# Performance work log

Measured on AMD Instinct MI355X. Metric: run time of the kernel, lower is better.

The kernel has to match this reference:

```python
import jax, jax.numpy as jnp
import numpy as np

B, N, KEY_DIM, VALUE_DIM, INNER_DIM, HEADS = 2, 4096, 512, 512, 512, 8
DIM_HEAD = INNER_DIM // HEADS
LN_EPS = 1e-5


def _layernorm(x, gamma, beta):
    mu = jnp.mean(x, axis=-1, keepdims=True)
    xc = x - mu
    var = jnp.mean(xc * xc, axis=-1, keepdims=True)
    return xc * jax.lax.rsqrt(var + LN_EPS) * gamma + beta


def setup_inputs() -> dict:
    key = jax.random.key(0)
    ks = jax.random.split(key, 8)
    keys = jax.random.normal(ks[0], (B, N, KEY_DIM), dtype=jnp.float32)
    values = jax.random.normal(ks[1], (B, N, VALUE_DIM), dtype=jnp.float32)
    mask = jax.random.randint(ks[2], (B, N), 0, 2).astype(jnp.bool_)
    W_qk = jax.random.normal(ks[3], (KEY_DIM, 2 * INNER_DIM), dtype=jnp.float32) * 0.02
    W_v = jax.random.normal(ks[4], (VALUE_DIM, INNER_DIM), dtype=jnp.float32) * 0.02
    W_out = jax.random.normal(ks[5], (INNER_DIM, VALUE_DIM), dtype=jnp.float32) * 0.02
    b_out = jnp.zeros((VALUE_DIM,), dtype=jnp.float32)
    qk_gamma = jnp.ones((KEY_DIM,), dtype=jnp.float32)
    qk_beta = jnp.zeros((KEY_DIM,), dtype=jnp.float32)
    v_gamma = jnp.ones((VALUE_DIM,), dtype=jnp.float32)
    v_beta = jnp.zeros((VALUE_DIM,), dtype=jnp.float32)
    return {"keys": keys, "values": values, "mask": mask,
            "qk_gamma": qk_gamma, "qk_beta": qk_beta,
            "v_gamma": v_gamma, "v_beta": v_beta,
            "W_qk": W_qk, "W_v": W_v, "W_out": W_out, "b_out": b_out}


def reference(keys, values, mask, qk_gamma, qk_beta, v_gamma, v_beta, W_qk, W_v, W_out, b_out):
    # LayerNorms on inputs
    kn = _layernorm(keys, qk_gamma, qk_beta)          # [B,N,KEY_DIM]
    vn = _layernorm(values, v_gamma, v_beta)          # [B,N,VALUE_DIM]
    # joint q/k projection, no bias
    qk = kn @ W_qk                                    # [B,N,2*INNER]
    q, k = qk[..., :INNER_DIM], qk[..., INNER_DIM:]
    # split heads: b n (h d) -> b h n d
    q = q.reshape(B, N, HEADS, DIM_HEAD).transpose(0, 2, 1, 3)
    k = k.reshape(B, N, HEADS, DIM_HEAD).transpose(0, 2, 1, 3)
    v = (vn @ W_v).reshape(B, N, HEADS, DIM_HEAD).transpose(0, 2, 1, 3)
    # clamp then scaled QK^T (AttentionMap math)
    q = jnp.clip(q, -5.0, 5.0)
    k = jnp.clip(k, -5.0, 5.0)
    scale = DIM_HEAD ** -0.5
    dots = jnp.einsum("bhqd,bhkd->bhqk", q, k) * scale  # [B,H,N,N]
    # mask: True keys are not attended to; broadcast (B,N)->(B,1,1,N)
    dots = jnp.where(mask[:, None, None, :], -jnp.inf, dots)
    attn = jax.nn.softmax(dots, axis=-1)
    out = jnp.einsum("bhqk,bhkd->bhqd", attn, v)       # [B,H,N,D]
    out = out.transpose(0, 2, 1, 3).reshape(B, N, INNER_DIM)
    return out @ W_out + b_out                         # [B,N,VALUE_DIM]
```

## Files before the change

### kernel.cpp

```cpp
#include <hip/hip_runtime.h>
#include <stdint.h>

typedef float f32x4 __attribute__((ext_vector_type(4)));
typedef float f32x16 __attribute__((ext_vector_type(16)));
typedef short s16x8 __attribute__((ext_vector_type(8)));
typedef int i32x4 __attribute__((ext_vector_type(4)));

typedef const __attribute__((address_space(1))) uint32_t* gas_t;
typedef __attribute__((address_space(3))) uint32_t* las_t;

__device__ __forceinline__ void gload16(const void* g, void* l) {
  __builtin_amdgcn_global_load_lds((gas_t)g, (las_t)l, 16, 0, 0);
}

__device__ __forceinline__ short f2bf(float f) {
  union { float f; uint32_t u; } v; v.f = f;
  uint32_t r = v.u + 0x7fffu + ((v.u >> 16) & 1u);
  return (short)(r >> 16);
}

__device__ __forceinline__ uint32_t cvtpk_bf16(float lo, float hi) {
  uint32_t r;
  asm("v_cvt_pk_bf16_f32 %0, %1, %2" : "=v"(r) : "v"(lo), "v"(hi));
  return r;
}

__device__ __forceinline__ void perm32swap(uint32_t& a, uint32_t& b) {
  asm("v_permlane32_swap_b32 %0, %1" : "+v"(a), "+v"(b));
}

#define MFMA16(a,b,c) __builtin_amdgcn_mfma_f32_16x16x32_bf16((a),(b),(c),0,0,0)
#define MFMA32(a,b,c) __builtin_amdgcn_mfma_f32_32x32x16_bf16((a),(b),(c),0,0,0)

__global__ __launch_bounds__(256) void prep_kernel(
    const uint32_t* __restrict__ maskp,
    const float* __restrict__ W_qk, const float* __restrict__ W_v,
    const float* __restrict__ W_out,
    short* __restrict__ WqkT, short* __restrict__ WvT, short* __restrict__ WoutT,
    const float* __restrict__ keys, const float* __restrict__ values,
    const float* __restrict__ g0, const float* __restrict__ b0,
    const float* __restrict__ g1, const float* __restrict__ b1,
    short* __restrict__ kn, short* __restrict__ vn,
    int* __restrict__ idx, int* __restrict__ cnts) {
  __shared__ float tile[32][33];
  __shared__ int wt[4];
  __shared__ int wdet[4];
  const int bid = blockIdx.x, t = threadIdx.x;
  const int lane = t & 63, w = t >> 6;

  if (bid < 2) {
    const int b = bid;
    uint4 probe = ((const uint4*)maskp)[t];
    bool big = (probe.x > 1u) || (probe.y > 1u) || (probe.z > 1u) || (probe.w > 1u);
    unsigned long long bal = __ballot(big);
    if (lane == 0) wdet[w] = (bal != 0ull) ? 1 : 0;
    __syncthreads();
    const int f = wdet[0] | wdet[1] | wdet[2] | wdet[3];

    int v[16]; int s = 0;
    if (f) {
      uint4 raw = ((const uint4*)((const uint8_t*)maskp + (size_t)b * 4096))[t];
      uint32_t ws_[4] = {raw.x, raw.y, raw.z, raw.w};
#pragma unroll
      for (int e = 0; e < 16; e++)
        v[e] = (((ws_[e >> 2] >> ((e & 3) * 8)) & 0xffu) == 0) ? 1 : 0;
    } else {
#pragma unroll
      for (int j = 0; j < 4; j++) {
        uint4 raw = ((const uint4*)(maskp + (size_t)b * 4096))[t * 4 + j];
        v[j * 4 + 0] = (raw.x == 0); v[j * 4 + 1] = (raw.y == 0);
        v[j * 4 + 2] = (raw.z == 0); v[j * 4 + 3] = (raw.w == 0);
      }
    }
#pragma unroll
    for (int e = 0; e < 16; e++) s += v[e];
    int sc = s;
#pragma unroll
    for (int off = 1; off < 64; off <<= 1) {
      int y = __shfl_up(sc, off);
      if (lane >= off) sc += y;
    }
    if (lane == 63) wt[w] = sc;
    __syncthreads();
    int woff = 0;
#pragma unroll
    for (int i = 0; i < 4; i++) if (i < w) woff += wt[i];
    int base = woff + sc - s;
#pragma unroll
    for (int e = 0; e < 16; e++)
      if (v[e]) { idx[b * 4096 + base] = b * 4096 + t * 16 + e; base++; }
    const int cnt = wt[0] + wt[1] + wt[2] + wt[3];
    const int cpad = (cnt + 127) & ~127;
    for (int j = cnt + t; j < cpad; j += 256) idx[b * 4096 + j] = 8192;
    if (t == 0) { cnts[b * 2] = cnt; cnts[b * 2 + 1] = cpad; }
  } else if (bid < 1026) {
    int job = bid - 2;
    const float* W; short* WT; int C;
    if (job < 512)       { W = W_qk;  WT = WqkT;  C = 1024; }
    else if (job < 768)  { job -= 512; W = W_v;   WT = WvT;  C = 512; }
    else                 { job -= 768; W = W_out; WT = WoutT; C = 512; }
    const int tx_ = C >> 5;
    const int c0 = (job % tx_) * 32, r0 = (job / tx_) * 32;
    const int tx = t & 31, ty = t >> 5;
#pragma unroll
    for (int i = 0; i < 32; i += 8)
      tile[ty + i][tx] = W[(size_t)(r0 + ty + i) * C + c0 + tx];
    __syncthreads();
#pragma unroll
    for (int i = 0; i < 32; i += 8)
      WT[(size_t)(c0 + ty + i) * 512 + r0 + tx] = f2bf(tile[tx][ty + i]);
  } else {
    int job = (bid - 1026) * 4 + w;
    if (job >= 16386) return;
    const int sel = job & 1, row = job >> 1;
    short* out = (sel ? vn : kn) + (size_t)row * 512;
    if (row == 8192) {
      s16x8 z = (s16x8){0,0,0,0,0,0,0,0};
      *(s16x8*)(out + lane * 8) = z;
      return;
    }
    const float* x = (sel ? values : keys) + (size_t)row * 512;
    const float* ga = sel ? g1 : g0;
    const float* be = sel ? b1 : b0;
    float4 a = ((const float4*)x)[lane * 2];
    float4 c = ((const float4*)x)[lane * 2 + 1];
    float s = a.x + a.y + a.z + a.w + c.x + c.y + c.z + c.w;
    float sq = a.x*a.x + a.y*a.y + a.z*a.z + a.w*a.w + c.x*c.x + c.y*c.y + c.z*c.z + c.w*c.w;
#pragma unroll
    for (int m = 1; m < 64; m <<= 1) { s += __shfl_xor(s, m); sq += __shfl_xor(sq, m); }
    float mu = s * (1.0f / 512.0f);
    float var = sq * (1.0f / 512.0f) - mu * mu;
    float rs = rsqrtf(var + 1e-5f);
    float xs[8] = {a.x, a.y, a.z, a.w, c.x, c.y, c.z, c.w};
    s16x8 o;
#pragma unroll
    for (int j = 0; j < 8; j++)
      o[j] = f2bf((xs[j] - mu) * rs * ga[lane * 8 + j] + be[lane * 8 + j]);
    *(s16x8*)(out + lane * 8) = o;
  }
}

__device__ __forceinline__ void gemm_core64(const short* __restrict__ A,
                                            const short* __restrict__ BT,
                                            int row0, int col0,
                                            short* ldsA, short* ldsB,
                                            f32x4 acc[4][2]) {
  const int t = threadIdx.x;
  const int lane = t & 63, w = t >> 6;
  const int wr = w >> 1, wc = w & 1;
  const int l15 = lane & 15, l4 = lane >> 4;
#pragma unroll
  for (int mi = 0; mi < 4; mi++)
#pragma unroll
    for (int ni = 0; ni < 2; ni++) acc[mi][ni] = (f32x4){0.f, 0.f, 0.f, 0.f};

  for (int k0 = 0; k0 < 512; k0 += 64) {
    __syncthreads();
#pragma unroll
    for (int i = 0; i < 4; i++) {
      int q = i * 256 + t;
      int row = q >> 3, ch = q & 7;
      int chs = ch ^ (row & 7);
      gload16(A + (size_t)(row0 + row) * 512 + k0 + chs * 8, ldsA + (i * 256 + w * 64) * 8);
    }
#pragma unroll
    for (int i = 0; i < 2; i++) {
      int q = i * 256 + t;
      int row = q >> 3, ch = q & 7;
      int chs = ch ^ (row & 7);
      gload16(BT + (size_t)(col0 + row) * 512 + k0 + chs * 8, ldsB + (i * 256 + w * 64) * 8);
    }
    __syncthreads();
#pragma unroll
    for (int kk = 0; kk < 2; kk++) {
      s16x8 af[4], bf[2];
#pragma unroll
      for (int mi = 0; mi < 4; mi++) {
        int row = wr * 64 + mi * 16 + l15;
        int ch = (kk * 4 + l4) ^ (row & 7);
        af[mi] = *(const s16x8*)(ldsA + row * 64 + ch * 8);
      }
#pragma unroll
      for (int ni = 0; ni < 2; ni++) {
        int row = wc * 32 + ni * 16 + l15;
        int ch = (kk * 4 + l4) ^ (row & 7);
        bf[ni] = *(const s16x8*)(ldsB + row * 64 + ch * 8);
      }
#pragma unroll
      for (int mi = 0; mi < 4; mi++)
#pragma unroll
        for (int ni = 0; ni < 2; ni++)
          acc[mi][ni] = MFMA16(af[mi], bf[ni], acc[mi][ni]);
    }
  }
}

__device__ __forceinline__ void gemm_core_idx(const short* __restrict__ A,
                                              const short* __restrict__ BT,
                                              const int* __restrict__ idxp,
                                              int row0, int col0,
                                              short* ldsA, short* ldsB,
                                              f32x4 acc[4][4]) {
  const int t = threadIdx.x;
  const int lane = t & 63, w = t >> 6;
  const int wr = w >> 1, wc = w & 1;
  const int l15 = lane & 15, l4 = lane >> 4;
  int arow[4];
#pragma unroll
  for (int i = 0; i < 4; i++)
    arow[i] = idxp[row0 + ((i * 256 + t) >> 3)];
#pragma unroll
  for (int mi = 0; mi < 4; mi++)
#pragma unroll
    for (int ni = 0; ni < 4; ni++) acc[mi][ni] = (f32x4){0.f, 0.f, 0.f, 0.f};

  for (int k0 = 0; k0 < 512; k0 += 64) {
    __syncthreads();
#pragma unroll
    for (int i = 0; i < 4; i++) {
      int q = i * 256 + t;
      int row = q >> 3, ch = q & 7;
      int chs = ch ^ (row & 7);
      gload16(A + (size_t)arow[i] * 512 + k0 + chs * 8, ldsA + (i * 256 + w * 64) * 8);
      gload16(BT + (size_t)(col0 + row) * 512 + k0 + chs * 8, ldsB + (i * 256 + w * 64) * 8);
    }
    __syncthreads();
#pragma unroll
    for (int kk = 0; kk < 2; kk++) {
      s16x8 af[4], bf[4];
#pragma unroll
      for (int mi = 0; mi < 4; mi++) {
        int row = wr * 64 + mi * 16 + l15;
        int ch = (kk * 4 + l4) ^ (row & 7);
        af[mi] = *(const s16x8*)(ldsA + row * 64 + ch * 8);
      }
#pragma unroll
      for (int ni = 0; ni < 4; ni++) {
        int row = wc * 64 + ni * 16 + l15;
        int ch = (kk * 4 + l4) ^ (row & 7);
        bf[ni] = *(const s16x8*)(ldsB + row * 64 + ch * 8);
      }
#pragma unroll
      for (int mi = 0; mi < 4; mi++)
#pragma unroll
        for (int ni = 0; ni < 4; ni++)
          acc[mi][ni] = MFMA16(af[mi], bf[ni], acc[mi][ni]);
    }
  }
}

__global__ __launch_bounds__(256) void proj_kernel(const short* __restrict__ kn,
    const short* __restrict__ vn, const short* __restrict__ WqkT,
    const short* __restrict__ WvT, const int* __restrict__ idx,
    const int* __restrict__ cnts, short* __restrict__ Qg,
    short* __restrict__ Kg, short* __restrict__ VTg) {
  __shared__ short lds[2][128 * 64];
  const int bid = blockIdx.x;
  const int t = threadIdx.x, lane = t & 63, w = t >> 6, wr = w >> 1, wc = w & 1;
  const int l15 = lane & 15, l4 = lane >> 4;

  if (bid < 512) {
    const int bm = bid >> 3, bn = bid & 7;
    f32x4 acc[4][2];
    gemm_core64(kn, WqkT, bm * 128, bn * 64, lds[0], lds[1], acc);
    const float QSCL = 0.125f * 1.44269504088896f;
#pragma unroll
    for (int mi = 0; mi < 4; mi++)
#pragma unroll
      for (int ni = 0; ni < 2; ni++) {
        int c = bn * 64 + wc * 32 + ni * 16 + l15;
        int h = c >> 6, d = c & 63;
#pragma unroll
        for (int r = 0; r < 4; r++) {
          int row = bm * 128 + wr * 64 + mi * 16 + l4 * 4 + r;
          int b = row >> 12, n = row & 4095;
          float v = acc[mi][ni][r];
          v = fminf(fmaxf(v, -5.0f), 5.0f) * QSCL;
          Qg[((size_t)((b * 8 + h) * 4096 + n) << 6) + d] = f2bf(v);
        }
      }
  } else {
    const int b2 = bid - 512;
    const int bm = b2 >> 4, bn = (b2 >> 2) & 3, z = b2 & 3;
    const int b = z & 1, isV = z >> 1;
    if (bm * 128 >= cnts[b * 2 + 1]) return;
    f32x4 acc[4][4];
    if (!isV) {
      gemm_core_idx(kn, WqkT, idx + b * 4096, bm * 128, 512 + bn * 128, lds[0], lds[1], acc);
#pragma unroll
      for (int mi = 0; mi < 4; mi++)
#pragma unroll
        for (int ni = 0; ni < 4; ni++) {
          int c = bn * 128 + wc * 64 + ni * 16 + l15;
          int h = c >> 6, d = c & 63;
#pragma unroll
          for (int r = 0; r < 4; r++) {
            int j = bm * 128 + wr * 64 + mi * 16 + l4 * 4 + r;
            float v = acc[mi][ni][r];
            v = fminf(fmaxf(v, -5.0f), 5.0f);
            Kg[((size_t)((b * 8 + h) * 4096 + j) << 6) + d] = f2bf(v);
          }
        }
    } else {
      gemm_core_idx(vn, WvT, idx + b * 4096, bm * 128, bn * 128, lds[0], lds[1], acc);
      __syncthreads();
      short* T = (short*)lds;
#pragma unroll
      for (int mi = 0; mi < 4; mi++)
#pragma unroll
        for (int ni = 0; ni < 4; ni++) {
          int c_loc = wc * 64 + ni * 16 + l15;
#pragma unroll
          for (int r = 0; r < 4; r++) {
            int n_loc = wr * 64 + mi * 16 + l4 * 4 + r;
            T[c_loc * 128 + (((n_loc >> 3) ^ (c_loc & 15)) << 3) + (n_loc & 7)] = f2bf(acc[mi][ni][r]);
          }
        }
      __syncthreads();
#pragma unroll
      for (int jj = 0; jj < 8; jj++) {
        int c_loc = jj * 16 + (t >> 4);
        int nch = t & 15;
        s16x8 v = *(const s16x8*)(T + c_loc * 128 + ((nch ^ (c_loc & 15)) << 3));
        int cg = bn * 128 + c_loc, h = cg >> 6, d = cg & 63;
        int j = bm * 128 + nch * 8;
        *(s16x8*)(VTg + (size_t)((b * 8 + h) * 64 + d) * 4096 + j) = v;
      }
    }
  }
}

__global__ __launch_bounds__(256) void gemm_out_kernel(const short* __restrict__ O,
    const short* __restrict__ WoutT, const float* __restrict__ bias, float* __restrict__ out) {
  __shared__ short ldsA[128 * 64], ldsB[64 * 64];
  f32x4 acc[4][2];
  const int bm = blockIdx.x, bn = blockIdx.y;
  gemm_core64(O, WoutT, bm * 128, bn * 64, ldsA, ldsB, acc);
  const int t = threadIdx.x, lane = t & 63, w = t >> 6, wr = w >> 1, wc = w & 1;
  const int l15 = lane & 15, l4 = lane >> 4;
#pragma unroll
  for (int ni = 0; ni < 2; ni++) {
    int col = bn * 64 + wc * 32 + ni * 16 + l15;
    float bv = bias[col];
#pragma unroll
    for (int mi = 0; mi < 4; mi++)
#pragma unroll
      for (int r = 0; r < 4; r++) {
        int row = bm * 128 + wr * 64 + mi * 16 + l4 * 4 + r;
        out[(size_t)row * 512 + col] = acc[mi][ni][r] + bv;
      }
  }
}

__global__ __launch_bounds__(512, 4) void attn_kernel(const short* __restrict__ Qg,
    const short* __restrict__ Kg, const short* __restrict__ VTg,
    const int* __restrict__ cnts, short* __restrict__ O) {
  __shared__ short smem[32768];
  short* KloB = smem;
  short* VloB = smem + 8192;
  short* KhiB = smem + 16384;
  short* VhiB = smem + 24576;

  const int bid = blockIdx.x;
  const int xcd = bid & 7, local = bid >> 3;
  const int bh = xcd * 2 + (local & 1);
  const int qb = local >> 1;
  const int b = bh >> 3, h = bh & 7;
  const int t = threadIdx.x, lane = t & 63, w = t >> 6;
  const int l31 = lane & 31, hh = lane >> 5;
  const int half = w >> 2, wq = w & 3;

  const short* Qp = Qg + (size_t)bh * 4096 * 64;
  const short* Kp = Kg + (size_t)bh * 4096 * 64;
  const short* Vp = VTg + (size_t)bh * 64 * 4096;

  const int cnt  = cnts[b * 2];
  const int cpad = cnts[b * 2 + 1];
  const int nit  = cpad >> 7;
  const int hb   = cpad >> 1;
  const int kbase = half ? hb : 0;

  const int qrow = qb * 128 + wq * 32 + l31;
  s16x8 qf[4];
#pragma unroll
  for (int dblk = 0; dblk < 4; dblk++)
    qf[dblk] = *(const s16x8*)(Qp + (size_t)qrow * 64 + dblk * 16 + hh * 8);

  f32x16 oac[2];
#pragma unroll
  for (int db = 0; db < 2; db++)
#pragma unroll
    for (int r = 0; r < 16; r++) oac[db][r] = 0.0f;
  float m_ = -60.0f, l_ = 0.0f;

  const short* KtS = half ? KhiB : KloB;
  const short* VtS = half ? VhiB : VloB;

  auto STAGE = [&](int buf, int i) {
    int row = t >> 3, ch = t & 7, chs = ch ^ (row & 7);
    gload16(Kp + (size_t)(i * 64 + row) * 64 + chs * 8,        KloB + buf * 4096 + w * 512);
    gload16(Kp + (size_t)(hb + i * 64 + row) * 64 + chs * 8,   KhiB + buf * 4096 + w * 512);
    gload16(Vp + (size_t)row * 4096 + i * 64 + chs * 8,        VloB + buf * 4096 + w * 512);
    gload16(Vp + (size_t)row * 4096 + hb + i * 64 + chs * 8,   VhiB + buf * 4096 + w * 512);
  };

  STAGE(0, 0);
  __syncthreads();

  for (int it = 0; it < nit; it++) {
    const int cur = it & 1;
    if (it < nit - 1) STAGE(cur ^ 1, it + 1);
    const short* Kt = KtS + cur * 4096;
    const int kb_t = kbase + it * 64;

    f32x16 sc[2];
    __builtin_amdgcn_s_setprio(1);
#pragma unroll
    for (int kb = 0; kb < 2; kb++) {
      f32x16 s_;
#pragma unroll
      for (int r = 0; r < 16; r++) s_[r] = 0.0f;
      const int krow = kb * 32 + l31;
#pragma unroll
      for (int dblk = 0; dblk < 4; dblk++) {
        int ch = (2 * dblk + hh) ^ (krow & 7);
        s16x8 kf = *(const s16x8*)(Kt + krow * 64 + ch * 8);
        s_ = MFMA32(kf, qf[dblk], s_);
      }
      sc[kb] = s_;
    }
    __builtin_amdgcn_s_setprio(0);

    if (kb_t + 64 > cnt) {
#pragma unroll
      for (int kb = 0; kb < 2; kb++)
#pragma unroll
        for (int r = 0; r < 16; r++) {
          int key = kb_t + kb * 32 + (r & 3) + 8 * (r >> 2) + 4 * hh;
          if (key >= cnt) sc[kb][r] = -1e30f;
        }
    }

    float mx0 = -1e30f, mx1 = -1e30f, mx2 = -1e30f, mx3 = -1e30f;
#pragma unroll
    for (int kb = 0; kb < 2; kb++)
#pragma unroll
      for (int r = 0; r < 16; r += 4) {
        mx0 = fmaxf(mx0, sc[kb][r + 0]);
        mx1 = fmaxf(mx1, sc[kb][r + 1]);
        mx2 = fmaxf(mx2, sc[kb][r + 2]);
        mx3 = fmaxf(mx3, sc[kb][r + 3]);
      }
    float mx = fmaxf(fmaxf(mx0, mx1), fmaxf(mx2, mx3));
    mx = fmaxf(mx, __shfl_xor(mx, 32));

    if (!__all(mx <= m_ + 5.0f)) {
      float mnew = fmaxf(m_, mx);
      float alpha = __builtin_amdgcn_exp2f(m_ - mnew);
      m_ = mnew;
      l_ *= alpha;
#pragma unroll
      for (int db = 0; db < 2; db++)
#pragma unroll
        for (int r = 0; r < 16; r++) oac[db][r] *= alpha;
    }

    float ls0 = 0.0f, ls1 = 0.0f, ls2 = 0.0f, ls3 = 0.0f;
    uint32_t pw[4][4];
#pragma unroll
    for (int kb = 0; kb < 2; kb++) {
      float p[16];
#pragma unroll
      for (int r = 0; r < 16; r += 4) {
        p[r + 0] = __builtin_amdgcn_exp2f(sc[kb][r + 0] - m_);
        p[r + 1] = __builtin_amdgcn_exp2f(sc[kb][r + 1] - m_);
        p[r + 2] = __builtin_amdgcn_exp2f(sc[kb][r + 2] - m_);
        p[r + 3] = __builtin_amdgcn_exp2f(sc[kb][r + 3] - m_);
        ls0 += p[r + 0]; ls1 += p[r + 1]; ls2 += p[r + 2]; ls3 += p[r + 3];
      }
#pragma unroll
      for (int ksl = 0; ksl < 2; ksl++) {
        const int fi = kb * 2 + ksl, b0 = ksl * 8;
        uint32_t a0 = cvtpk_bf16(p[b0 + 0], p[b0 + 1]);
        uint32_t b0w = cvtpk_bf16(p[b0 + 4], p[b0 + 5]);
        perm32swap(a0, b0w);
        uint32_t a1 = cvtpk_bf16(p[b0 + 2], p[b0 + 3]);
        uint32_t b1w = cvtpk_bf16(p[b0 + 6], p[b0 + 7]);
        perm32swap(a1, b1w);
        pw[fi][0] = a0; pw[fi][1] = a1; pw[fi][2] = b0w; pw[fi][3] = b1w;
      }
    }
    float ls = (ls0 + ls1) + (ls2 + ls3);
    ls += __shfl_xor(ls, 32);
    l_ += ls;

    __builtin_amdgcn_s_setprio(1);
#pragma unroll
    for (int db = 0; db < 2; db++) {
      const int d = db * 32 + l31;
#pragma unroll
      for (int ks = 0; ks < 4; ks++) {
        int ch = (2 * ks + hh) ^ (d & 7);
        s16x8 vf = *(const s16x8*)(VtS + cur * 4096 + d * 64 + ch * 8);
        i32x4 pv = {(int)pw[ks][0], (int)pw[ks][1], (int)pw[ks][2], (int)pw[ks][3]};
        oac[db] = MFMA32(vf, __builtin_bit_cast(s16x8, pv), oac[db]);
      }
    }
    __builtin_amdgcn_s_setprio(0);

    __syncthreads();
  }

  float* mrg = (float*)smem;
  float* ml  = mrg + 8192;
  if (half) {
#pragma unroll
    for (int db = 0; db < 2; db++)
#pragma unroll
      for (int r = 0; r < 16; r++)
        mrg[wq * 2048 + (db * 16 + r) * 64 + lane] = oac[db][r];
    ml[wq * 128 + lane * 2]     = m_;
    ml[wq * 128 + lane * 2 + 1] = l_;
  }
  __syncthreads();
  if (!half) {
    float m2 = ml[wq * 128 + lane * 2];
    float l2 = ml[wq * 128 + lane * 2 + 1];
    float mF = fmaxf(m_, m2);
    float e1 = __builtin_amdgcn_exp2f(m_ - mF);
    float e2 = __builtin_amdgcn_exp2f(m2 - mF);
    l_ = l_ * e1 + l2 * e2;
#pragma unroll
    for (int db = 0; db < 2; db++)
#pragma unroll
      for (int r = 0; r < 16; r++)
        oac[db][r] = oac[db][r] * e1 + mrg[wq * 2048 + (db * 16 + r) * 64 + lane] * e2;

    float inv = 1.0f / l_;
    short* epi = smem + 17408 + wq * 2048;
#pragma unroll
    for (int db = 0; db < 2; db++)
#pragma unroll
      for (int g = 0; g < 4; g++) {
        uint32_t w0 = cvtpk_bf16(oac[db][g * 4 + 0] * inv, oac[db][g * 4 + 1] * inv);
        uint32_t w1 = cvtpk_bf16(oac[db][g * 4 + 2] * inv, oac[db][g * 4 + 3] * inv);
        int chunk = db * 4 + g;
        uint2* dst = (uint2*)((char*)epi + l31 * 128 + ((chunk ^ (l31 & 7)) << 4) + hh * 8);
        *dst = make_uint2(w0, w1);
      }
#pragma unroll
    for (int i = 0; i < 4; i++) {
      int c = hh * 4 + i;
      s16x8 v = *(const s16x8*)((char*)epi + l31 * 128 + ((c ^ (l31 & 7)) << 4));
      *(s16x8*)(O + ((size_t)(b * 4096 + qrow) * 512) + h * 64 + c * 8) = v;
    }
  }
}

extern "C" void kernel_launch(void* const* d_in, const int* in_sizes, int n_in,
                              void* d_out, int out_size, void* d_ws, size_t ws_size,
                              hipStream_t stream) {
  const float* keys     = (const float*)d_in[0];
  const float* values   = (const float*)d_in[1];
  const uint32_t* maskp = (const uint32_t*)d_in[2];
  const float* qk_gamma = (const float*)d_in[3];
  const float* qk_beta  = (const float*)d_in[4];
  const float* v_gamma  = (const float*)d_in[5];
  const float* v_beta   = (const float*)d_in[6];
  const float* W_qk     = (const float*)d_in[7];
  const float* W_v      = (const float*)d_in[8];
  const float* W_out    = (const float*)d_in[9];
  const float* b_out    = (const float*)d_in[10];
  float* out = (float*)d_out;
  char* ws = (char*)d_ws;
  const size_t MB = 1u << 20;
  short* kn    = (short*)(ws);
  short* vn    = (short*)(ws + 9 * MB);
  short* Qg    = (short*)(ws + 18 * MB);
  short* Kg    = (short*)(ws + 26 * MB);
  short* VTg   = (short*)(ws + 34 * MB);
  short* O     = (short*)(ws + 42 * MB);
  short* WqkT  = (short*)(ws + 50 * MB);
  short* WvT   = (short*)(ws + 51 * MB);
  short* WoutT = (short*)(ws + 51 * MB + 512 * 1024);
  int*   idx   = (int*)(ws + 52 * MB);
  int*   cnts  = (int*)(ws + 52 * MB + 32 * 1024);

  prep_kernel<<<5123, 256, 0, stream>>>(maskp, W_qk, W_v, W_out, WqkT, WvT, WoutT,
                                        keys, values, qk_gamma, qk_beta, v_gamma, v_beta,
                                        kn, vn, idx, cnts);
  proj_kernel<<<1024, 256, 0, stream>>>(kn, vn, WqkT, WvT, idx, cnts, Qg, Kg, VTg);
  attn_kernel<<<512, 512, 0, stream>>>(Qg, Kg, VTg, cnts, O);
  gemm_out_kernel<<<dim3(64, 8), 256, 0, stream>>>(O, WoutT, b_out, out);
}
```

Measured before the change: 95.53 us.

## Halve attention key tile per iteration to shrink LDS and raise occupancy

Each attention iteration now stages 32 keys per half (one 32-key MFMA block per wave-half) instead of 64. The K and V staging is packed into one shared buffer pair, cutting shared memory from 64KB to about 34KB. The launch bound is raised from 4 to 8 blocks per CU. The aim is more resident blocks and lower LDS pressure. The cost is twice as many loop iterations and barriers, and a tighter register budget that may cause spills.

```diff
diff --git a/kernel.cpp b/kernel.cpp
--- a/kernel.cpp
+++ b/kernel.cpp
@@ -352,14 +352,12 @@
   }
 }
 
-__global__ __launch_bounds__(512, 4) void attn_kernel(const short* __restrict__ Qg,
+__global__ __launch_bounds__(512, 8) void attn_kernel(const short* __restrict__ Qg,
     const short* __restrict__ Kg, const short* __restrict__ VTg,
     const int* __restrict__ cnts, short* __restrict__ O) {
-  __shared__ short smem[32768];
-  short* KloB = smem;
-  short* VloB = smem + 8192;
-  short* KhiB = smem + 16384;
-  short* VhiB = smem + 24576;
+  __shared__ short smem[17408];
+  short* KtB = smem;
+  short* VtB = smem + 8192;
 
   const int bid = blockIdx.x;
   const int xcd = bid & 7, local = bid >> 3;
@@ -376,7 +374,7 @@
 
   const int cnt  = cnts[b * 2];
   const int cpad = cnts[b * 2 + 1];
-  const int nit  = cpad >> 7;
+  const int nit  = cpad >> 6;
   const int hb   = cpad >> 1;
   const int kbase = half ? hb : 0;
 
@@ -393,15 +391,16 @@
     for (int r = 0; r < 16; r++) oac[db][r] = 0.0f;
   float m_ = -60.0f, l_ = 0.0f;
 
-  const short* KtS = half ? KhiB : KloB;
-  const short* VtS = half ? VhiB : VloB;
-
   auto STAGE = [&](int buf, int i) {
     int row = t >> 3, ch = t & 7, chs = ch ^ (row & 7);
-    gload16(Kp + (size_t)(i * 64 + row) * 64 + chs * 8,        KloB + buf * 4096 + w * 512);
-    gload16(Kp + (size_t)(hb + i * 64 + row) * 64 + chs * 8,   KhiB + buf * 4096 + w * 512);
-    gload16(Vp + (size_t)row * 4096 + i * 64 + chs * 8,        VloB + buf * 4096 + w * 512);
-    gload16(Vp + (size_t)row * 4096 + hb + i * 64 + chs * 8,   VhiB + buf * 4096 + w * 512);
+    const short* ksrc = (row < 32)
+        ? Kp + (size_t)(i * 32 + row) * 64 + chs * 8
+        : Kp + (size_t)(hb + i * 32 + row - 32) * 64 + chs * 8;
+    gload16(ksrc, KtB + buf * 4096 + w * 512);
+    const short* vsrc = (chs < 4)
+        ? Vp + (size_t)row * 4096 + i * 32 + chs * 8
+        : Vp + (size_t)row * 4096 + hb + i * 32 + (chs - 4) * 8;
+    gload16(vsrc, VtB + buf * 4096 + w * 512);
   };
 
   STAGE(0, 0);
@@ -410,47 +409,36 @@
   for (int it = 0; it < nit; it++) {
     const int cur = it & 1;
     if (it < nit - 1) STAGE(cur ^ 1, it + 1);
-    const short* Kt = KtS + cur * 4096;
-    const int kb_t = kbase + it * 64;
-
-    f32x16 sc[2];
+    const short* Kt = KtB + cur * 4096;
+    const int kb_t = kbase + it * 32;
+
+    f32x16 sc;
+#pragma unroll
+    for (int r = 0; r < 16; r++) sc[r] = 0.0f;
+    const int krow = half * 32 + l31;
     __builtin_amdgcn_s_setprio(1);
 #pragma unroll
-    for (int kb = 0; kb < 2; kb++) {
-      f32x16 s_;
-#pragma unroll
-      for (int r = 0; r < 16; r++) s_[r] = 0.0f;
-      const int krow = kb * 32 + l31;
-#pragma unroll
-      for (int dblk = 0; dblk < 4; dblk++) {
-        int ch = (2 * dblk + hh) ^ (krow & 7);
-        s16x8 kf = *(const s16x8*)(Kt + krow * 64 + ch * 8);
-        s_ = MFMA32(kf, qf[dblk], s_);
-      }
-      sc[kb] = s_;
+    for (int dblk = 0; dblk < 4; dblk++) {
+      int ch = (2 * dblk + hh) ^ (krow & 7);
+      s16x8 kf = *(const s16x8*)(Kt + krow * 64 + ch * 8);
+      sc = MFMA32(kf, qf[dblk], sc);
     }
     __builtin_amdgcn_s_setprio(0);
 
-    if (kb_t + 64 > cnt) {
-#pragma unroll
-      for (int kb = 0; kb < 2; kb++)
-#pragma unroll
-        for (int r = 0; r < 16; r++) {
-          int key = kb_t + kb * 32 + (r & 3) + 8 * (r >> 2) + 4 * hh;
-          if (key >= cnt) sc[kb][r] = -1e30f;
-        }
-    }
-
-    float mx0 = -1e30f, mx1 = -1e30f, mx2 = -1e30f, mx3 = -1e30f;
-#pragma unroll
-    for (int kb = 0; kb < 2; kb++)
-#pragma unroll
-      for (int r = 0; r < 16; r += 4) {
-        mx0 = fmaxf(mx0, sc[kb][r + 0]);
-        mx1 = fmaxf(mx1, sc[kb][r + 1]);
-        mx2 = fmaxf(mx2, sc[kb][r + 2]);
-        mx3 = fmaxf(mx3, sc[kb][r + 3]);
-      }
+    if (kb_t + 32 > cnt) {
+#pragma unroll
+      for (int r = 0; r < 16; r++) {
+        int key = kb_t + (r & 3) + 8 * (r >> 2) + 4 * hh;
+        if (key >= cnt) sc[r] = -1e30f;
+      }
+    }
+
+    float mx0 = fmaxf(sc[0], sc[4]),  mx1 = fmaxf(sc[1], sc[5]);
+    float mx2 = fmaxf(sc[2], sc[6]),  mx3 = fmaxf(sc[3], sc[7]);
+    mx0 = fmaxf(mx0, fmaxf(sc[8], sc[12]));
+    mx1 = fmaxf(mx1, fmaxf(sc[9], sc[13]));
+    mx2 = fmaxf(mx2, fmaxf(sc[10], sc[14]));
+    mx3 = fmaxf(mx3, fmaxf(sc[11], sc[15]));
     float mx = fmaxf(fmaxf(mx0, mx1), fmaxf(mx2, mx3));
     mx = fmaxf(mx, __shfl_xor(mx, 32));
 
@@ -466,29 +454,26 @@
     }
 
     float ls0 = 0.0f, ls1 = 0.0f, ls2 = 0.0f, ls3 = 0.0f;
-    uint32_t pw[4][4];
-#pragma unroll
-    for (int kb = 0; kb < 2; kb++) {
-      float p[16];
-#pragma unroll
-      for (int r = 0; r < 16; r += 4) {
-        p[r + 0] = __builtin_amdgcn_exp2f(sc[kb][r + 0] - m_);
-        p[r + 1] = __builtin_amdgcn_exp2f(sc[kb][r + 1] - m_);
-        p[r + 2] = __builtin_amdgcn_exp2f(sc[kb][r + 2] - m_);
-        p[r + 3] = __builtin_amdgcn_exp2f(sc[kb][r + 3] - m_);
-        ls0 += p[r + 0]; ls1 += p[r + 1]; ls2 += p[r + 2]; ls3 += p[r + 3];
-      }
-#pragma unroll
-      for (int ksl = 0; ksl < 2; ksl++) {
-        const int fi = kb * 2 + ksl, b0 = ksl * 8;
-        uint32_t a0 = cvtpk_bf16(p[b0 + 0], p[b0 + 1]);
-        uint32_t b0w = cvtpk_bf16(p[b0 + 4], p[b0 + 5]);
-        perm32swap(a0, b0w);
-        uint32_t a1 = cvtpk_bf16(p[b0 + 2], p[b0 + 3]);
-        uint32_t b1w = cvtpk_bf16(p[b0 + 6], p[b0 + 7]);
-        perm32swap(a1, b1w);
-        pw[fi][0] = a0; pw[fi][1] = a1; pw[fi][2] = b0w; pw[fi][3] = b1w;
-      }
+    float p[16];
+#pragma unroll
+    for (int r = 0; r < 16; r += 4) {
+      p[r + 0] = __builtin_amdgcn_exp2f(sc[r + 0] - m_);
+      p[r + 1] = __builtin_amdgcn_exp2f(sc[r + 1] - m_);
+      p[r + 2] = __builtin_amdgcn_exp2f(sc[r + 2] - m_);
+      p[r + 3] = __builtin_amdgcn_exp2f(sc[r + 3] - m_);
+      ls0 += p[r + 0]; ls1 += p[r + 1]; ls2 += p[r + 2]; ls3 += p[r + 3];
+    }
+    uint32_t pw[2][4];
+#pragma unroll
+    for (int ksl = 0; ksl < 2; ksl++) {
+      const int b0 = ksl * 8;
+      uint32_t a0 = cvtpk_bf16(p[b0 + 0], p[b0 + 1]);
+      uint32_t b0w = cvtpk_bf16(p[b0 + 4], p[b0 + 5]);
+      perm32swap(a0, b0w);
+      uint32_t a1 = cvtpk_bf16(p[b0 + 2], p[b0 + 3]);
+      uint32_t b1w = cvtpk_bf16(p[b0 + 6], p[b0 + 7]);
+      perm32swap(a1, b1w);
+      pw[ksl][0] = a0; pw[ksl][1] = a1; pw[ksl][2] = b0w; pw[ksl][3] = b1w;
     }
     float ls = (ls0 + ls1) + (ls2 + ls3);
     ls += __shfl_xor(ls, 32);
@@ -496,14 +481,16 @@
 
     __builtin_amdgcn_s_setprio(1);
 #pragma unroll
-    for (int db = 0; db < 2; db++) {
-      const int d = db * 32 + l31;
-#pragma unroll
-      for (int ks = 0; ks < 4; ks++) {
-        int ch = (2 * ks + hh) ^ (d & 7);
-        s16x8 vf = *(const s16x8*)(VtS + cur * 4096 + d * 64 + ch * 8);
-        i32x4 pv = {(int)pw[ks][0], (int)pw[ks][1], (int)pw[ks][2], (int)pw[ks][3]};
-        oac[db] = MFMA32(vf, __builtin_bit_cast(s16x8, pv), oac[db]);
+    for (int ksl = 0; ksl < 2; ksl++) {
+      i32x4 pv = {(int)pw[ksl][0], (int)pw[ksl][1], (int)pw[ksl][2], (int)pw[ksl][3]};
+      s16x8 pf = __builtin_bit_cast(s16x8, pv);
+      const int ks_g = half * 2 + ksl;
+#pragma unroll
+      for (int db = 0; db < 2; db++) {
+        const int d = db * 32 + l31;
+        int ch = (2 * ks_g + hh) ^ (d & 7);
+        s16x8 vf = *(const s16x8*)(VtB + cur * 4096 + d * 64 + ch * 8);
+        oac[db] = MFMA32(vf, pf, oac[db]);
       }
     }
     __builtin_amdgcn_s_setprio(0);
@@ -512,7 +499,7 @@
   }
 
   float* mrg = (float*)smem;
-  float* ml  = mrg + 8192;
+  float* ml  = (float*)(smem + 16384);
   if (half) {
 #pragma unroll
     for (int db = 0; db < 2; db++)
@@ -537,7 +524,7 @@
         oac[db][r] = oac[db][r] * e1 + mrg[wq * 2048 + (db * 16 + r) * 64 + lane] * e2;
 
     float inv = 1.0f / l_;
-    short* epi = smem + 17408 + wq * 2048;
+    short* epi = smem + wq * 4096;
 #pragma unroll
     for (int db = 0; db < 2; db++)
 #pragma unroll
```

New measurement: 200.4 us. +109.7%, slower.
